# Kernel tuning notes

Hardware: AMD Instinct MI355X
Metric: run time of the kernel (lower is better)

## Reference

```python
import jax, jax.numpy as jnp
import numpy as np

B, N, DIM_IN, DIM_K, DIM_V, NH = 2, 2048, 1024, 1024, 1024, 16

def setup_inputs() -> dict:
    key = jax.random.key(0)
    ks = jax.random.split(key, 7)
    s_in = 1.0 / np.sqrt(DIM_IN)
    return {
        "x": jax.random.normal(ks[0], (B, N, DIM_IN), dtype=jnp.float32),
        "Wq": jax.random.uniform(ks[1], (DIM_IN, DIM_K), jnp.float32, -s_in, s_in),
        "bq": jax.random.uniform(ks[2], (DIM_K,), jnp.float32, -s_in, s_in),
        "Wk": jax.random.uniform(ks[3], (DIM_IN, DIM_K), jnp.float32, -s_in, s_in),
        "bk": jax.random.uniform(ks[4], (DIM_K,), jnp.float32, -s_in, s_in),
        "Wv": jax.random.uniform(ks[5], (DIM_IN, DIM_V), jnp.float32, -s_in, s_in),
        "bv": jax.random.uniform(ks[6], (DIM_V,), jnp.float32, -s_in, s_in),
    }

def reference(x, Wq, bq, Wk, bk, Wv, bv):
    b, n, _ = x.shape
    dk = DIM_K // NH
    dv = DIM_V // NH
    scale = 1.0 / np.sqrt(dk)
    # project and split heads: [b, nh, n, dk]
    q = (x @ Wq + bq).reshape(b, n, NH, dk).transpose(0, 2, 1, 3)
    k = (x @ Wk + bk).reshape(b, n, NH, dk).transpose(0, 2, 1, 3)
    v = (x @ Wv + bv).reshape(b, n, NH, dv).transpose(0, 2, 1, 3)
    dist = jnp.einsum('bhqd,bhkd->bhqk', q, k) * scale  # [b,nh,n,n]
    dist = jax.nn.softmax(dist, axis=-1)
    att = jnp.einsum('bhqk,bhkd->bhqd', dist, v)
    return att.transpose(0, 2, 1, 3).reshape(b, n, DIM_V)
```

## Files before the change

kernel.cpp:

```cpp
#include <hip/hip_runtime.h>

#define DI __device__ __forceinline__

typedef unsigned short u16;
typedef short short8 __attribute__((ext_vector_type(8)));
typedef float f32x2 __attribute__((ext_vector_type(2)));
typedef float f32x4 __attribute__((ext_vector_type(4)));
typedef float f32x16 __attribute__((ext_vector_type(16)));
typedef u16 u16x4 __attribute__((ext_vector_type(4)));
typedef unsigned u32x4 __attribute__((ext_vector_type(4)));
typedef int i32x2 __attribute__((ext_vector_type(2)));

DI u16 f2bf(float f){
    unsigned u = __builtin_bit_cast(unsigned, f);
    u += 0x7FFFu + ((u >> 16) & 1u);
    return (u16)(u >> 16);
}
DI float bf2f(u16 b){
    unsigned u = ((unsigned)b) << 16;
    return __builtin_bit_cast(float, u);
}

#if defined(__has_builtin)
#if __has_builtin(__builtin_amdgcn_global_load_lds)
#define HAS_GLL 1
#endif
#if __has_builtin(__builtin_amdgcn_exp2f)
#define HAS_EXP2 1
#endif
#if __has_builtin(__builtin_amdgcn_permlane32_swap)
#define HAS_PL32 1
#endif
#endif

DI void async16(u16* lds, const u16* g){
#ifdef HAS_GLL
    __builtin_amdgcn_global_load_lds(
        (const __attribute__((address_space(1))) unsigned int*)g,
        (__attribute__((address_space(3))) unsigned int*)lds, 16, 0, 0);
#else
    *(short8*)lds = *(const short8*)g;
#endif
}

DI float ex2(float x){
#ifdef HAS_EXP2
    return __builtin_amdgcn_exp2f(x);
#else
    return exp2f(x);
#endif
}

DI unsigned cvtpk(float lo, float hi){
    unsigned r;
    asm("v_cvt_pk_bf16_f32 %0, %1, %2" : "=v"(r) : "v"(lo), "v"(hi));
    return r;
}

DI i32x2 plswap(int a, int b){
#ifdef HAS_PL32
    return __builtin_amdgcn_permlane32_swap(a, b, false, false);
#else
    i32x2 r;
    int ax = __shfl_xor(a, 32), bx = __shfl_xor(b, 32);
    int hi = (threadIdx.x & 63) >> 5;
    r[0] = hi ? bx : a;
    r[1] = hi ? b : ax;
    return r;
#endif
}

#define SEQ   2048
#define DIN   1024
#define MTOT  4096
#define QSCALE 0.18033688011112042f

__global__ void k_prep(const float* __restrict__ x,
                       const float* __restrict__ Wq, const float* __restrict__ Wk,
                       const float* __restrict__ Wv,
                       u16* __restrict__ xb, u16* __restrict__ Wt3){
    __shared__ float t[32][33];
    int bid = blockIdx.x, tid = threadIdx.x;
    if (bid < 4096){
        int i = (bid * 256 + tid) * 4;
        f32x4 v = *(const f32x4*)(x + i);
        u16x4 o;
        #pragma unroll
        for (int j = 0; j < 4; j++) o[j] = f2bf(v[j]);
        *(u16x4*)(xb + i) = o;
    } else {
        int tb = bid - 4096;
        int z  = tb >> 10;
        int t2 = tb & 1023;
        const float* W = (z == 0) ? Wq : (z == 1) ? Wk : Wv;
        u16* Wt = Wt3 + (size_t)z * DIN * DIN;
        int tx = tid & 31, ty = tid >> 5;
        int n0 = (t2 & 31) * 32, k0 = (t2 >> 5) * 32;
        #pragma unroll
        for (int i = 0; i < 4; i++)
            t[ty + i*8][tx] = W[(size_t)(k0 + ty + i*8) * DIN + n0 + tx];
        __syncthreads();
        #pragma unroll
        for (int i = 0; i < 4; i++)
            Wt[(size_t)(n0 + ty + i*8) * DIN + k0 + tx] = f2bf(t[tx][ty + i*8]);
    }
}

__global__ __launch_bounds__(256, 3) void k_projf(const u16* __restrict__ A,
                                                  const u16* __restrict__ Wt3,
                                                  const float* __restrict__ bq,
                                                  const float* __restrict__ bk,
                                                  const float* __restrict__ bv,
                                                  u16* __restrict__ qb,
                                                  u16* __restrict__ kb,
                                                  u16* __restrict__ vtb){
    __shared__ __align__(16) u16 As[2][4096];
    __shared__ __align__(16) u16 Bs[2][4096];
    int tid = threadIdx.x;
    int l = tid & 63, w = tid >> 6;
    int lq = l & 15, lg = l >> 4;
    int wm = w >> 1, wn = w & 1;
    int by  = blockIdx.y;
    int mat = by >> 3;
    int m0 = blockIdx.x * 128, n0 = (by & 7) * 128;
    const u16* Bt = Wt3 + (size_t)mat * DIN * DIN;
    const float* bias = (mat == 0) ? bq : (mat == 1) ? bk : bv;

    int r0 = tid >> 2, c0 = (tid & 3) * 8;
    const u16* ap0 = A  + (size_t)(m0 + r0)      * DIN + c0;
    const u16* ap1 = A  + (size_t)(m0 + 64 + r0) * DIN + c0;
    const u16* bp0 = Bt + (size_t)(n0 + r0)      * DIN + c0;
    const u16* bp1 = Bt + (size_t)(n0 + 64 + r0) * DIN + c0;
    int d0 = tid * 8, d1 = 2048 + tid * 8;

#define PSTAGE(bi) {                                              \
    async16(&As[bi][d0], ap0); async16(&As[bi][d1], ap1);         \
    async16(&Bs[bi][d0], bp0); async16(&Bs[bi][d1], bp1);         \
    ap0 += 32; ap1 += 32; bp0 += 32; bp1 += 32; }

    f32x4 acc[4][4] = {};
    PSTAGE(0)

    for (int t = 0; t < 32; t++){
        int cur = t & 1;
        if (t + 1 < 32) PSTAGE(cur ^ 1)
        if (t == 0){
            asm volatile("s_waitcnt vmcnt(4)" ::: "memory");
            __builtin_amdgcn_s_barrier();
        }

        short8 af[4], bf[4];
        #pragma unroll
        for (int f = 0; f < 4; f++){
            af[f] = *(const short8*)&As[cur][(wm*64 + f*16 + lq) * 32 + lg * 8];
            bf[f] = *(const short8*)&Bs[cur][(wn*64 + f*16 + lq) * 32 + lg * 8];
        }
        __builtin_amdgcn_s_setprio(1);
        #pragma unroll
        for (int fm = 0; fm < 4; fm++)
            #pragma unroll
            for (int fn = 0; fn < 4; fn++)
                acc[fm][fn] = __builtin_amdgcn_mfma_f32_16x16x32_bf16(af[fm], bf[fn], acc[fm][fn], 0, 0, 0);
        __builtin_amdgcn_s_setprio(0);

        asm volatile("s_waitcnt vmcnt(0)" ::: "memory");
        __builtin_amdgcn_s_barrier();
    }
#undef PSTAGE

    if (mat == 2){
        for (int fn = 0; fn < 4; fn++){
            int cc = n0 + wn*64 + fn*16 + lq;
            float bvv = bias[cc];
            int hh = cc >> 6, d = cc & 63;
            for (int fm = 0; fm < 4; fm++){
                int mbase = m0 + wm*64 + fm*16 + lg*4;
                int b = mbase >> 11, n = mbase & 2047;
                u16x4 pv;
                for (int r = 0; r < 4; r++) pv[r] = f2bf(acc[fm][fn][r] + bvv);
                *(u16x4*)&vtb[((size_t)(b*16 + hh) * 64 + d) * SEQ + n] = pv;
            }
        }
    } else {
        u16* dst = (mat == 0) ? qb : kb;
        float sc = (mat == 0) ? QSCALE : 1.0f;
        u16* Cs = &As[0][0];
        float bvv[4];
        #pragma unroll
        for (int fn = 0; fn < 4; fn++) bvv[fn] = bias[n0 + wn*64 + fn*16 + lq];

        for (int fm = 0; fm < 4; fm++){
            __syncthreads();
            #pragma unroll
            for (int fn = 0; fn < 4; fn++){
                int c = wn*64 + fn*16 + lq;
                #pragma unroll
                for (int r = 0; r < 4; r++)
                    Cs[(wm*16 + lg*4 + r)*136 + c] = f2bf((acc[fm][fn][r] + bvv[fn]) * sc);
            }
            __syncthreads();
            #pragma unroll
            for (int j = 0; j < 2; j++){
                int wr = (tid >> 4) + j*16;
                int coloff = (tid & 15) * 8;
                int ng = m0 + (wr >> 4)*64 + fm*16 + (wr & 15);
                int b = ng >> 11, n = ng & 2047;
                int cg = n0 + coloff;
                int hh = cg >> 6, d = cg & 63;
                *(short8*)&dst[((size_t)(b*16 + hh) * SEQ + n) * 64 + d] =
                    *(const short8*)&Cs[wr*136 + coloff];
            }
        }
    }
}

#define MFMA32(a, b, c) __builtin_amdgcn_mfma_f32_32x32x16_bf16(a, b, c, 0, 0, 0)

#define MAKE_PA(dst, S, base) {                                   \
    unsigned a0 = cvtpk(S[base+0], S[base+1]);                    \
    unsigned a1 = cvtpk(S[base+2], S[base+3]);                    \
    unsigned b0 = cvtpk(S[base+4], S[base+5]);                    \
    unsigned b1 = cvtpk(S[base+6], S[base+7]);                    \
    i32x2 r0 = plswap((int)a0, (int)b0);                          \
    i32x2 r1 = plswap((int)a1, (int)b1);                          \
    u32x4 wv = {(unsigned)r0[0], (unsigned)r1[0],                 \
                (unsigned)r0[1], (unsigned)r1[1]};                \
    dst = __builtin_bit_cast(short8, wv); }

template<int SPLIT>
__global__ __launch_bounds__(256, 5) void k_attn(const u16* __restrict__ Q,
                                                 const u16* __restrict__ K,
                                                 const u16* __restrict__ Vt,
                                                 float* __restrict__ out,
                                                 u16* __restrict__ po,
                                                 float* __restrict__ mls){
    __shared__ __align__(16) u16 Ks[2][4096];
    __shared__ __align__(16) u16 Vs[2][4096];

    int tid = threadIdx.x, l = tid & 63, w = tid >> 6;
    int lq = l & 31, hi = l >> 5;

    int bid = (blockIdx.z * 32 + blockIdx.y) * 16 + blockIdx.x;
    const int nwg = 512 * SPLIT;
    int d = (bid & 7) * (nwg >> 3) + (bid >> 3);
    const int perbh = 16 * SPLIT;
    int bh = d / perbh;
    int rem = d - bh * perbh;
    int sp = rem >> 4;
    int qx = rem & 15;

    int b = bh >> 4, h = bh & 15;
    int q0 = qx * 128 + w * 32;
    int kvb = sp * (SEQ / SPLIT);
    const int NT = (SEQ / SPLIT) / 64;

    const u16* Qb = Q  + (size_t)bh * SEQ * 64;
    const u16* Kb = K  + (size_t)bh * SEQ * 64;
    const u16* Vb = Vt + (size_t)bh * 64 * SEQ;

    int row0 = tid >> 3;
    int c0   = (tid & 7) ^ (row0 & 7);
    const u16* kp0 = Kb + (size_t)(kvb + row0)      * 64 + c0 * 8;
    const u16* kp1 = Kb + (size_t)(kvb + row0 + 32) * 64 + c0 * 8;
    const u16* vp0 = Vb + (size_t)row0        * SEQ + kvb + c0 * 8;
    const u16* vp1 = Vb + (size_t)(row0 + 32) * SEQ + kvb + c0 * 8;
    int d0 = tid * 8, d1 = 2048 + tid * 8;

#define STAGE(bi) {                                               \
    async16(&Ks[bi][d0], kp0); async16(&Ks[bi][d1], kp1);         \
    async16(&Vs[bi][d0], vp0); async16(&Vs[bi][d1], vp1);         \
    kp0 += 64*64; kp1 += 64*64; vp0 += 64; vp1 += 64; }

    short8 qf[4];
    #pragma unroll
    for (int ks = 0; ks < 4; ks++)
        qf[ks] = *(const short8*)(Qb + (size_t)(q0 + lq) * 64 + ks*16 + hi*8);

    STAGE(0)

    float m = 0.f;
    float ls = 0.f;
    f32x16 o0 = {}, o1 = {};
    int rx = (lq & 7) << 4;

    for (int t = 0; t < NT; t++){
        int cur = t & 1;
        if (t + 1 < NT) STAGE(cur ^ 1)
        if (t == 0){
            if (NT > 1) asm volatile("s_waitcnt vmcnt(4)" ::: "memory");
            else        asm volatile("s_waitcnt vmcnt(0)" ::: "memory");
            __builtin_amdgcn_s_barrier();
        }

        const char* kB = (const char*)&Ks[cur][0];
        const char* vB = (const char*)&Vs[cur][0];

        f32x16 st0 = {}, st1 = {};
        __builtin_amdgcn_s_setprio(1);
        #pragma unroll
        for (int ks = 0; ks < 4; ks++){
            int cb = ((ks*2 + hi) << 4) ^ rx;
            short8 ka = *(const short8*)(kB + lq*128        + cb);
            short8 kb = *(const short8*)(kB + (32+lq)*128   + cb);
            st0 = MFMA32(ka, qf[ks], st0);
            st1 = MFMA32(kb, qf[ks], st1);
        }
        __builtin_amdgcn_s_setprio(0);

        if (m != 0.f){
            #pragma unroll
            for (int r = 0; r < 16; r++){ st0[r] -= m; st1[r] -= m; }
        }

        f32x2 ps = {0.f, 0.f};
        #pragma unroll
        for (int r = 0; r < 16; r += 2){
            st0[r]   = ex2(st0[r]);
            st0[r+1] = ex2(st0[r+1]);
            st1[r]   = ex2(st1[r]);
            st1[r+1] = ex2(st1[r+1]);
            f32x2 a = {st0[r], st0[r+1]};
            f32x2 c = {st1[r], st1[r+1]};
            ps += a + c;
        }
        float psum = ps[0] + ps[1];
        psum += __shfl_xor(psum, 32);

        short8 pa0, pa1, pa2, pa3;
        MAKE_PA(pa0, st0, 0)
        MAKE_PA(pa1, st0, 8)
        MAKE_PA(pa2, st1, 0)
        MAKE_PA(pa3, st1, 8)

        __builtin_amdgcn_s_setprio(1);
        #pragma unroll
        for (int kct = 0; kct < 4; kct++){
            short8 pf = (kct == 0) ? pa0 : (kct == 1) ? pa1 : (kct == 2) ? pa2 : pa3;
            int cb = ((kct*2 + hi) << 4) ^ rx;
            short8 v0 = *(const short8*)(vB + lq*128      + cb);
            short8 v1 = *(const short8*)(vB + (32+lq)*128 + cb);
            o0 = MFMA32(pf, v0, o0);
            o1 = MFMA32(pf, v1, o1);
        }
        __builtin_amdgcn_s_setprio(0);

        ls += psum;
        if (__any(ls > 1.0e30f)){
            const float dn = 5.421010862427522e-20f;
            ls *= dn;
            #pragma unroll
            for (int r = 0; r < 16; r++){ o0[r] *= dn; o1[r] *= dn; }
            m += 64.f;
        }

        asm volatile("s_waitcnt vmcnt(0)" ::: "memory");
        __builtin_amdgcn_s_barrier();
    }

    if (SPLIT == 1){
        #pragma unroll
        for (int r = 0; r < 16; r++){
            int row = (r & 3) + 8*(r >> 2) + 4*hi;
            float inv = 1.0f / __shfl(ls, row);
            float* op = out + ((size_t)b * SEQ + (q0 + row)) * 1024 + h*64 + lq;
            op[0]  = o0[r] * inv;
            op[32] = o1[r] * inv;
        }
    } else {
        u16* pb = po + (size_t)sp * MTOT * 1024;
        #pragma unroll
        for (int r = 0; r < 16; r++){
            int row = (r & 3) + 8*(r >> 2) + 4*hi;
            u16* op = pb + ((size_t)b * SEQ + (q0 + row)) * 1024 + h*64 + lq;
            op[0]  = f2bf(o0[r]);
            op[32] = f2bf(o1[r]);
        }
        if (hi == 0){
            float* mp = mls + (((size_t)sp*32 + bh) * SEQ + (q0 + lq)) * 2;
            mp[0] = m; mp[1] = ls;
        }
    }
#undef STAGE
}

template<int S>
__global__ __launch_bounds__(256) void k_comb(const u16* __restrict__ po,
                                              const float* __restrict__ mls,
                                              float* __restrict__ out){
    size_t i = ((size_t)blockIdx.x * 256 + threadIdx.x) * 4;
    size_t row = i >> 10;
    int col = (int)(i & 1023);
    int b = (int)(row >> 11), n = (int)(row & 2047);
    int bh = b*16 + (col >> 6);

    float mv[S], lv[S], wv[S];
    float M = -INFINITY;
    #pragma unroll
    for (int s = 0; s < S; s++){
        const float* p = mls + (((size_t)s*32 + bh) * SEQ + n) * 2;
        mv[s] = p[0]; lv[s] = p[1];
        M = fmaxf(M, mv[s]);
    }
    float L = 0.f;
    #pragma unroll
    for (int s = 0; s < S; s++){ wv[s] = ex2(mv[s] - M); L += wv[s] * lv[s]; }
    float inv = 1.0f / L;
    f32x4 acc = {};
    #pragma unroll
    for (int s = 0; s < S; s++){
        u16x4 v = *(const u16x4*)(po + (size_t)s * MTOT * 1024 + i);
        #pragma unroll
        for (int j = 0; j < 4; j++) acc[j] += wv[s] * bf2f(v[j]);
    }
    acc *= inv;
    *(f32x4*)(out + i) = acc;
}

extern "C" void kernel_launch(void* const* d_in, const int* in_sizes, int n_in,
                              void* d_out, int out_size, void* d_ws, size_t ws_size,
                              hipStream_t stream){
    const float* x  = (const float*)d_in[0];
    const float* Wq = (const float*)d_in[1];
    const float* bq = (const float*)d_in[2];
    const float* Wk = (const float*)d_in[3];
    const float* bk = (const float*)d_in[4];
    const float* Wv = (const float*)d_in[5];
    const float* bv = (const float*)d_in[6];
    float* out = (float*)d_out;

    const size_t MB = (size_t)1 << 20;
    if (ws_size < 38 * MB) return;

    char* ws = (char*)d_ws;
    u16* xb   = (u16*)(ws);
    u16* wt3  = (u16*)(ws +  8 * MB);
    u16* qb   = (u16*)(ws + 14 * MB);
    u16* kb   = (u16*)(ws + 22 * MB);
    u16* vtb  = (u16*)(ws + 30 * MB);
    int S = 1;
    if      (ws_size >= 38 * MB + 4 * 9 * MB) S = 4;
    else if (ws_size >= 38 * MB + 2 * 9 * MB) S = 2;
    u16* po    = (u16*)(ws + 38 * MB);
    float* mls = (float*)(ws + 38 * MB + (size_t)S * 8 * MB);

    k_prep<<<7168, 256, 0, stream>>>(x, Wq, Wk, Wv, xb, wt3);

    k_projf<<<dim3(32, 24), 256, 0, stream>>>(xb, wt3, bq, bk, bv, qb, kb, vtb);

    if (S == 4){
        k_attn<4><<<dim3(16, 32, 4), 256, 0, stream>>>(qb, kb, vtb, out, po, mls);
        k_comb<4><<<4096, 256, 0, stream>>>(po, mls, out);
    } else if (S == 2){
        k_attn<2><<<dim3(16, 32, 2), 256, 0, stream>>>(qb, kb, vtb, out, po, mls);
        k_comb<2><<<4096, 256, 0, stream>>>(po, mls, out);
    } else {
        k_attn<1><<<dim3(16, 32, 1), 256, 0, stream>>>(qb, kb, vtb, out, po, mls);
    }
}
```

Measured before the change: 114.1 us.

## Load K fragments directly from global memory and cap KV split at two

K tiles are no longer staged through LDS; each lane reads its K MFMA operand straight from global memory while only V stays double-buffered in shared memory. This halves LDS use and drops the swizzled LDS reads for K, at the cost of uncoalesced, latency-exposed global loads inside the QK loop. The occupancy hint drops from 5 to 4 blocks per CU. The split-KV factor is limited to 2, which trades less combine work and partial-output traffic for fewer blocks in flight.

```diff
diff --git a/kernel.cpp b/kernel.cpp
--- a/kernel.cpp
+++ b/kernel.cpp
@@ -228,13 +228,12 @@
     dst = __builtin_bit_cast(short8, wv); }
 
 template<int SPLIT>
-__global__ __launch_bounds__(256, 5) void k_attn(const u16* __restrict__ Q,
+__global__ __launch_bounds__(256, 4) void k_attn(const u16* __restrict__ Q,
                                                  const u16* __restrict__ K,
                                                  const u16* __restrict__ Vt,
                                                  float* __restrict__ out,
                                                  u16* __restrict__ po,
                                                  float* __restrict__ mls){
-    __shared__ __align__(16) u16 Ks[2][4096];
     __shared__ __align__(16) u16 Vs[2][4096];
 
     int tid = threadIdx.x, l = tid & 63, w = tid >> 6;
@@ -260,23 +259,23 @@
 
     int row0 = tid >> 3;
     int c0   = (tid & 7) ^ (row0 & 7);
-    const u16* kp0 = Kb + (size_t)(kvb + row0)      * 64 + c0 * 8;
-    const u16* kp1 = Kb + (size_t)(kvb + row0 + 32) * 64 + c0 * 8;
     const u16* vp0 = Vb + (size_t)row0        * SEQ + kvb + c0 * 8;
     const u16* vp1 = Vb + (size_t)(row0 + 32) * SEQ + kvb + c0 * 8;
     int d0 = tid * 8, d1 = 2048 + tid * 8;
 
-#define STAGE(bi) {                                               \
-    async16(&Ks[bi][d0], kp0); async16(&Ks[bi][d1], kp1);         \
+#define STAGEV(bi) {                                              \
     async16(&Vs[bi][d0], vp0); async16(&Vs[bi][d1], vp1);         \
-    kp0 += 64*64; kp1 += 64*64; vp0 += 64; vp1 += 64; }
+    vp0 += 64; vp1 += 64; }
 
     short8 qf[4];
     #pragma unroll
     for (int ks = 0; ks < 4; ks++)
         qf[ks] = *(const short8*)(Qb + (size_t)(q0 + lq) * 64 + ks*16 + hi*8);
 
-    STAGE(0)
+    const u16* kl0 = Kb + (size_t)(kvb + lq)      * 64 + hi * 8;
+    const u16* kl1 = Kb + (size_t)(kvb + 32 + lq) * 64 + hi * 8;
+
+    STAGEV(0)
 
     float m = 0.f;
     float ls = 0.f;
@@ -285,27 +284,24 @@
 
     for (int t = 0; t < NT; t++){
         int cur = t & 1;
-        if (t + 1 < NT) STAGE(cur ^ 1)
-        if (t == 0){
-            if (NT > 1) asm volatile("s_waitcnt vmcnt(4)" ::: "memory");
-            else        asm volatile("s_waitcnt vmcnt(0)" ::: "memory");
-            __builtin_amdgcn_s_barrier();
-        }
-
-        const char* kB = (const char*)&Ks[cur][0];
-        const char* vB = (const char*)&Vs[cur][0];
+        if (t + 1 < NT) STAGEV(cur ^ 1)
 
         f32x16 st0 = {}, st1 = {};
         __builtin_amdgcn_s_setprio(1);
         #pragma unroll
         for (int ks = 0; ks < 4; ks++){
-            int cb = ((ks*2 + hi) << 4) ^ rx;
-            short8 ka = *(const short8*)(kB + lq*128        + cb);
-            short8 kb = *(const short8*)(kB + (32+lq)*128   + cb);
+            short8 ka = *(const short8*)(kl0 + ks*16);
+            short8 kb = *(const short8*)(kl1 + ks*16);
             st0 = MFMA32(ka, qf[ks], st0);
             st1 = MFMA32(kb, qf[ks], st1);
         }
         __builtin_amdgcn_s_setprio(0);
+        kl0 += 64*64; kl1 += 64*64;
+
+        if (t == 0){
+            asm volatile("s_waitcnt vmcnt(0)" ::: "memory");
+            __builtin_amdgcn_s_barrier();
+        }
 
         if (m != 0.f){
             #pragma unroll
@@ -332,6 +328,7 @@
         MAKE_PA(pa2, st1, 0)
         MAKE_PA(pa3, st1, 8)
 
+        const char* vB = (const char*)&Vs[cur][0];
         __builtin_amdgcn_s_setprio(1);
         #pragma unroll
         for (int kct = 0; kct < 4; kct++){
@@ -380,7 +377,7 @@
             mp[0] = m; mp[1] = ls;
         }
     }
-#undef STAGE
+#undef STAGEV
 }
 
 template<int S>
@@ -437,9 +434,7 @@
     u16* qb   = (u16*)(ws + 14 * MB);
     u16* kb   = (u16*)(ws + 22 * MB);
     u16* vtb  = (u16*)(ws + 30 * MB);
-    int S = 1;
-    if      (ws_size >= 38 * MB + 4 * 9 * MB) S = 4;
-    else if (ws_size >= 38 * MB + 2 * 9 * MB) S = 2;
+    int S = (ws_size >= 38 * MB + 2 * 9 * MB) ? 2 : 1;
     u16* po    = (u16*)(ws + 38 * MB);
     float* mls = (float*)(ws + 38 * MB + (size_t)S * 8 * MB);
 
@@ -447,10 +442,7 @@
 
     k_projf<<<dim3(32, 24), 256, 0, stream>>>(xb, wt3, bq, bk, bv, qb, kb, vtb);
 
-    if (S == 4){
-        k_attn<4><<<dim3(16, 32, 4), 256, 0, stream>>>(qb, kb, vtb, out, po, mls);
-        k_comb<4><<<4096, 256, 0, stream>>>(po, mls, out);
-    } else if (S == 2){
+    if (S == 2){
         k_attn<2><<<dim3(16, 32, 2), 256, 0, stream>>>(qb, kb, vtb, out, po, mls);
         k_comb<2><<<4096, 256, 0, stream>>>(po, mls, out);
     } else {
```

After: 118.3 us. 3.7% more time.
